# Kernel tuning notes

Hardware: AMD Instinct MI355X
Metric: run time of the kernel (lower is better)

## Reference

```python
import math
import jax, jax.numpy as jnp
import numpy as np

B, N, DQ, DK, DV, H = 8, 1024, 256, 256, 256, 8
EPS_SM = 1e-15
EPS_LN = 1e-5


def _layer_norm(x, g, b):
    mu = jnp.mean(x, axis=-1, keepdims=True)
    var = jnp.mean((x - mu) ** 2, axis=-1, keepdims=True)
    return (x - mu) * jax.lax.rsqrt(var + EPS_LN) * g + b


def setup_inputs() -> dict:
    key = jax.random.key(0)
    ks = jax.random.split(key, 16)
    s = 0.05
    inp = {
        "Q": jax.random.normal(ks[0], (B, N, DQ), jnp.float32),
        "K": jax.random.normal(ks[1], (B, N, DK), jnp.float32),
        "lengths": jnp.clip(jax.random.randint(ks[2], (B,), 0, N), 1, N),
        "Wq": jax.random.normal(ks[3], (DQ, DV), jnp.float32) * s,
        "bq": jnp.zeros((DV,), jnp.float32),
        "Wk": jax.random.normal(ks[4], (DK, DV), jnp.float32) * s,
        "bk": jnp.zeros((DV,), jnp.float32),
        "Wv": jax.random.normal(ks[5], (DK, DV), jnp.float32) * s,
        "bv": jnp.zeros((DV,), jnp.float32),
        "Wo": jax.random.normal(ks[6], (DV, DV), jnp.float32) * s,
        "bo": jnp.zeros((DV,), jnp.float32),
        "g0": jnp.ones((DV,), jnp.float32),
        "b0": jnp.zeros((DV,), jnp.float32),
        "g1": jnp.ones((DV,), jnp.float32),
        "b1": jnp.zeros((DV,), jnp.float32),
    }
    return inp


def reference(Q, K, lengths, Wq, bq, Wk, bk, Wv, bv, Wo, bo, g0, b0, g1, b1):
    d = DV // H  # head dim
    mask = (jnp.arange(N) < lengths[:, None]).astype(Q.dtype)  # (B, N)
    q = (Q @ Wq + bq) * mask[..., None]  # (B, N, DV)
    k = (K @ Wk + bk) * mask[..., None]
    v = (K @ Wv + bv) * mask[..., None]
    qh = q.reshape(B, N, H, d)
    kh = k.reshape(B, N, H, d)
    vh = v.reshape(B, N, H, d)
    # NB: original scales by sqrt(dim_V), not sqrt(head_dim)
    scores = jnp.einsum("bnhd,bmhd->bhnm", qh, kh) / math.sqrt(DV)
    # set_softmax: raw exp, mask rows and cols by lengths, normalize over keys
    e = jnp.exp(scores) * mask[:, None, :, None] * mask[:, None, None, :]
    A = e / (jnp.sum(e, axis=-1, keepdims=True) + EPS_SM)  # (B, H, N, N)
    O = qh + jnp.einsum("bhnm,bmhd->bnhd", A, vh)  # residual per head
    O = O.reshape(B, N, DV)
    O = _layer_norm(O, g0, b0)
    O = O + jax.nn.relu(O @ Wo + bo)
    O = _layer_norm(O, g1, b1)
    return O
```

## Files before the change

kernel.cpp:

```cpp
#include <hip/hip_runtime.h>
#include <hip/hip_bf16.h>


typedef __attribute__((ext_vector_type(8))) short short8;
typedef __attribute__((ext_vector_type(4))) short short4v;
typedef __attribute__((ext_vector_type(4))) float f32x4;

__device__ __forceinline__ short f2bf(float f) {
    union { float f; unsigned u; } x; x.f = f;
    unsigned r = x.u + 0x7fffu + ((x.u >> 16) & 1u);
    return (short)(r >> 16);
}
__device__ __forceinline__ float bf2f(short s) {
    union { unsigned u; float f; } x; x.u = ((unsigned)(unsigned short)s) << 16;
    return x.f;
}

__global__ __launch_bounds__(256) void wtrans_kernel(
    const float* __restrict__ Wq, const float* __restrict__ Wk,
    const float* __restrict__ Wv, const float* __restrict__ Wo,
    short* __restrict__ WqT, short* __restrict__ WkT,
    short* __restrict__ WvT, short* __restrict__ WoT)
{
    const float* W; short* T;
    switch (blockIdx.y) {
        case 0:  W = Wq; T = WqT; break;
        case 1:  W = Wk; T = WkT; break;
        case 2:  W = Wv; T = WvT; break;
        default: W = Wo; T = WoT; break;
    }
    int base = blockIdx.x * 4096 + threadIdx.x;
    #pragma unroll
    for (int i = 0; i < 16; i++) {
        int e = base + i * 256;
        int n = e >> 8, k = e & 255;
        T[e] = f2bf(W[k * 256 + n]);
    }
}

__global__ __launch_bounds__(256) void proj_kernel(
    const float* __restrict__ Q, const float* __restrict__ Kin,
    const short* __restrict__ WqT, const short* __restrict__ WkT, const short* __restrict__ WvT,
    const float* __restrict__ bq, const float* __restrict__ bk, const float* __restrict__ bv,
    const int* __restrict__ lengths,
    short* __restrict__ qb, short* __restrict__ kb, short* __restrict__ vT)
{
    const int which = blockIdx.y;
    const float* A    = (which == 0) ? Q   : Kin;
    const short* WT   = (which == 0) ? WqT : (which == 1) ? WkT : WvT;
    const float* bias = (which == 0) ? bq  : (which == 1) ? bk  : bv;

    const int tid = threadIdx.x;
    const int lane = tid & 63, wid = tid >> 6;
    const int m = lane & 15, quad = lane >> 4;
    const int rh = wid >> 1, ch = wid & 1;
    const int r0 = blockIdx.x * 32 + rh * 16;
    const int c0 = ch * 128;
    const int b = blockIdx.x >> 5;
    const int len = lengths[b];
    const int ntok0 = r0 & 1023;

    f32x4 acc[8];
    #pragma unroll
    for (int t = 0; t < 8; t++) acc[t] = (f32x4){0.f, 0.f, 0.f, 0.f};

    if (ntok0 < len) {
        const float* arow = A + (size_t)(r0 + m) * 256;
        for (int kk = 0; kk < 256; kk += 32) {
            const float* ap = arow + kk + quad * 8;
            float4 f0 = *(const float4*)(ap);
            float4 f1 = *(const float4*)(ap + 4);
            short8 af;
            af[0] = f2bf(f0.x); af[1] = f2bf(f0.y); af[2] = f2bf(f0.z); af[3] = f2bf(f0.w);
            af[4] = f2bf(f1.x); af[5] = f2bf(f1.y); af[6] = f2bf(f1.z); af[7] = f2bf(f1.w);
            #pragma unroll
            for (int t = 0; t < 8; t++) {
                short8 bf = *(const short8*)(WT + (c0 + t * 16 + m) * 256 + kk + quad * 8);
                acc[t] = __builtin_amdgcn_mfma_f32_16x16x32_bf16(af, bf, acc[t], 0, 0, 0);
            }
        }
    }

    #pragma unroll
    for (int t = 0; t < 8; t++) {
        int n = c0 + t * 16 + m;
        float bv_ = bias[n];
        int h = n >> 5, i = n & 31;
        int bh = b * 8 + h;
        #pragma unroll
        for (int reg = 0; reg < 4; reg++) {
            int ntok = ntok0 + quad * 4 + reg;
            float val = (ntok < len) ? (acc[t][reg] + bv_) : 0.f;
            short s = f2bf(val);
            if (which == 2) {
                vT[(size_t)(bh * 32 + i) * 1024 + ntok] = s;
            } else {
                short* dst = (which == 0) ? qb : kb;
                dst[((size_t)bh * 1024 + ntok) * 32 + i] = s;
            }
        }
    }
}

__global__ __launch_bounds__(256) void attn_kernel(
    const short* __restrict__ qb, const short* __restrict__ kb, const short* __restrict__ vT,
    const int* __restrict__ lengths, float* __restrict__ O1)
{
    __shared__ short P[4][16][72];
    __shared__ float cbO[2][16][33];
    __shared__ float cbL[2][16];
    const int tid = threadIdx.x;
    const int lane = tid & 63, wid = tid >> 6;
    const int m = lane & 15, quad = lane >> 4;
    const int ks = wid & 1, qh = wid >> 1;
    const int bh = blockIdx.y;
    const int b = bh >> 3, h = bh & 7;
    const int len = lengths[b];
    const int qr0 = blockIdx.x * 32 + qh * 16;

    const short* qbase = qb + (size_t)bh * 1024 * 32;
    const short* kbase = kb + (size_t)bh * 1024 * 32;
    const short* vbase = vT + (size_t)bh * 32 * 1024;

    const short8 qf = *(const short8*)(qbase + (qr0 + m) * 32 + quad * 8);

    f32x4 o0 = (f32x4){0.f, 0.f, 0.f, 0.f};
    f32x4 o1 = (f32x4){0.f, 0.f, 0.f, 0.f};
    float l[4] = {0.f, 0.f, 0.f, 0.f};

    const int kbeg = ks * 512;
    int kchunks = 0;
    if (qr0 < len && len > kbeg) {
        int rem = len - kbeg;
        kchunks = rem >= 512 ? 8 : ((rem + 63) >> 6);
    }

    for (int ci = 0; ci < kchunks; ci++) {
        int key0 = kbeg + ci * 64;
        #pragma unroll
        for (int t = 0; t < 4; t++) {
            short8 kf = *(const short8*)(kbase + (key0 + t * 16 + m) * 32 + quad * 8);
            f32x4 s = __builtin_amdgcn_mfma_f32_16x16x32_bf16(qf, kf,
                        (f32x4){0.f, 0.f, 0.f, 0.f}, 0, 0, 0);
            int col = key0 + t * 16 + m;
            bool cm = col < len;
            #pragma unroll
            for (int reg = 0; reg < 4; reg++) {
                float e = cm ? __expf(s[reg] * 0.0625f) : 0.f;
                l[reg] += e;
                P[wid][quad * 4 + reg][t * 16 + m] = f2bf(e);
            }
        }
        asm volatile("s_waitcnt lgkmcnt(0)" ::: "memory");
        #pragma unroll
        for (int c = 0; c < 2; c++) {
            short8 pf  = *(const short8*)(&P[wid][m][c * 32 + quad * 8]);
            short8 vf0 = *(const short8*)(vbase + (size_t)(m) * 1024      + key0 + c * 32 + quad * 8);
            short8 vf1 = *(const short8*)(vbase + (size_t)(16 + m) * 1024 + key0 + c * 32 + quad * 8);
            o0 = __builtin_amdgcn_mfma_f32_16x16x32_bf16(pf, vf0, o0, 0, 0, 0);
            o1 = __builtin_amdgcn_mfma_f32_16x16x32_bf16(pf, vf1, o1, 0, 0, 0);
        }
    }

    #pragma unroll
    for (int reg = 0; reg < 4; reg++) {
        float s = l[reg];
        s += __shfl_xor(s, 1); s += __shfl_xor(s, 2);
        s += __shfl_xor(s, 4); s += __shfl_xor(s, 8);
        l[reg] = s;
    }

    if (ks == 1) {
        #pragma unroll
        for (int reg = 0; reg < 4; reg++) {
            cbO[qh][quad * 4 + reg][m]      = o0[reg];
            cbO[qh][quad * 4 + reg][16 + m] = o1[reg];
        }
        if (m == 0) {
            #pragma unroll
            for (int reg = 0; reg < 4; reg++) cbL[qh][quad * 4 + reg] = l[reg];
        }
    }
    __syncthreads();
    if (ks == 0) {
        const int hbase = h * 32;
        #pragma unroll
        for (int reg = 0; reg < 4; reg++) {
            int r = quad * 4 + reg;
            o0[reg] += cbO[qh][r][m];
            o1[reg] += cbO[qh][r][16 + m];
            float lt = l[reg] + cbL[qh][r];
            int qrow = qr0 + r;
            float f = (qrow < len) ? 1.f / (lt + 1e-15f) : 0.f;
            size_t obase = ((size_t)(b * 1024 + qrow)) * 256 + hbase;
            float q0 = bf2f(qbase[qrow * 32 + m]);
            float q1 = bf2f(qbase[qrow * 32 + 16 + m]);
            O1[obase + m]      = q0 + o0[reg] * f;
            O1[obase + 16 + m] = q1 + o1[reg] * f;
        }
    }
}

__global__ __launch_bounds__(256) void ln0_kernel(
    const float* __restrict__ O1, const float* __restrict__ g0, const float* __restrict__ b0,
    short* __restrict__ Xb)
{
    const int tid = threadIdx.x;
    const int lane = tid & 63, wid = tid >> 6;
    const int token = blockIdx.x * 4 + wid;
    const float* row = O1 + (size_t)token * 256;
    float4 x = *(const float4*)(row + lane * 4);
    float s  = x.x + x.y + x.z + x.w;
    float s2 = x.x * x.x + x.y * x.y + x.z * x.z + x.w * x.w;
    #pragma unroll
    for (int msk = 1; msk < 64; msk <<= 1) {
        s  += __shfl_xor(s, msk);
        s2 += __shfl_xor(s2, msk);
    }
    float mean = s * (1.f / 256.f);
    float var  = s2 * (1.f / 256.f) - mean * mean;
    float rs = rsqrtf(var + 1e-5f);
    float4 g = *(const float4*)(g0 + lane * 4);
    float4 bb = *(const float4*)(b0 + lane * 4);
    short4v y;
    y[0] = f2bf((x.x - mean) * rs * g.x + bb.x);
    y[1] = f2bf((x.y - mean) * rs * g.y + bb.y);
    y[2] = f2bf((x.z - mean) * rs * g.z + bb.z);
    y[3] = f2bf((x.w - mean) * rs * g.w + bb.w);
    *(short4v*)(Xb + (size_t)token * 256 + lane * 4) = y;
}

__global__ __launch_bounds__(256) void out_kernel(
    const short* __restrict__ Xb, const short* __restrict__ WoT,
    const float* __restrict__ bo, const float* __restrict__ g1, const float* __restrict__ b1,
    float* __restrict__ out)
{
    __shared__ float st[2][2][2][16];
    const int tid = threadIdx.x;
    const int lane = tid & 63, wid = tid >> 6;
    const int m = lane & 15, quad = lane >> 4;
    const int rh = wid >> 1, ch = wid & 1;
    const int r0 = blockIdx.x * 32 + rh * 16;
    const int c0 = ch * 128;

    f32x4 acc[8];
    #pragma unroll
    for (int t = 0; t < 8; t++) acc[t] = (f32x4){0.f, 0.f, 0.f, 0.f};

    const short* arow = Xb + (size_t)(r0 + m) * 256;
    for (int kk = 0; kk < 256; kk += 32) {
        short8 af = *(const short8*)(arow + kk + quad * 8);
        #pragma unroll
        for (int t = 0; t < 8; t++) {
            short8 bf = *(const short8*)(WoT + (c0 + t * 16 + m) * 256 + kk + quad * 8);
            acc[t] = __builtin_amdgcn_mfma_f32_16x16x32_bf16(af, bf, acc[t], 0, 0, 0);
        }
    }

    float s1[4] = {0.f, 0.f, 0.f, 0.f};
    float s2[4] = {0.f, 0.f, 0.f, 0.f};
    #pragma unroll
    for (int t = 0; t < 8; t++) {
        int n = c0 + t * 16 + m;
        float bon = bo[n];
        #pragma unroll
        for (int reg = 0; reg < 4; reg++) {
            int token = r0 + quad * 4 + reg;
            float xv = bf2f(Xb[(size_t)token * 256 + n]);
            float c = acc[t][reg] + bon;
            float yv = xv + (c > 0.f ? c : 0.f);
            acc[t][reg] = yv;
            s1[reg] += yv;
            s2[reg] += yv * yv;
        }
    }
    #pragma unroll
    for (int reg = 0; reg < 4; reg++) {
        float a = s1[reg], bsum = s2[reg];
        a += __shfl_xor(a, 1); a += __shfl_xor(a, 2); a += __shfl_xor(a, 4); a += __shfl_xor(a, 8);
        bsum += __shfl_xor(bsum, 1); bsum += __shfl_xor(bsum, 2); bsum += __shfl_xor(bsum, 4); bsum += __shfl_xor(bsum, 8);
        s1[reg] = a; s2[reg] = bsum;
    }
    if (m == 0) {
        #pragma unroll
        for (int reg = 0; reg < 4; reg++) {
            st[rh][ch][0][quad * 4 + reg] = s1[reg];
            st[rh][ch][1][quad * 4 + reg] = s2[reg];
        }
    }
    __syncthreads();
    #pragma unroll
    for (int reg = 0; reg < 4; reg++) {
        int r = quad * 4 + reg;
        float t1 = s1[reg] + st[rh][ch ^ 1][0][r];
        float t2 = s2[reg] + st[rh][ch ^ 1][1][r];
        float mean = t1 * (1.f / 256.f);
        float var  = t2 * (1.f / 256.f) - mean * mean;
        float rs = rsqrtf(var + 1e-5f);
        int token = r0 + r;
        #pragma unroll
        for (int t = 0; t < 8; t++) {
            int n = c0 + t * 16 + m;
            out[(size_t)token * 256 + n] = (acc[t][reg] - mean) * rs * g1[n] + b1[n];
        }
    }
}

extern "C" void kernel_launch(void* const* d_in, const int* in_sizes, int n_in,
                              void* d_out, int out_size, void* d_ws, size_t ws_size,
                              hipStream_t stream) {
    const float* Q   = (const float*)d_in[0];
    const float* K   = (const float*)d_in[1];
    const int* lengths = (const int*)d_in[2];
    const float* Wq  = (const float*)d_in[3];
    const float* bq  = (const float*)d_in[4];
    const float* Wk  = (const float*)d_in[5];
    const float* bk  = (const float*)d_in[6];
    const float* Wv  = (const float*)d_in[7];
    const float* bv  = (const float*)d_in[8];
    const float* Wo  = (const float*)d_in[9];
    const float* bo  = (const float*)d_in[10];
    const float* g0  = (const float*)d_in[11];
    const float* b0  = (const float*)d_in[12];
    const float* g1  = (const float*)d_in[13];
    const float* b1  = (const float*)d_in[14];
    float* out = (float*)d_out;

    char* ws = (char*)d_ws;
    short* qb  = (short*)(ws);
    short* kb  = (short*)(ws + (4u << 20));
    short* vT  = (short*)(ws + (8u << 20));
    float* O1  = (float*)(ws + (12u << 20));
    short* Xb  = (short*)(ws + (20u << 20));
    short* WqT = (short*)(ws + (24u << 20));
    short* WkT = (short*)(ws + (24u << 20) + (128u << 10));
    short* WvT = (short*)(ws + (24u << 20) + (256u << 10));
    short* WoT = (short*)(ws + (24u << 20) + (384u << 10));

    wtrans_kernel<<<dim3(16, 4), 256, 0, stream>>>(Wq, Wk, Wv, Wo, WqT, WkT, WvT, WoT);
    proj_kernel<<<dim3(256, 3), 256, 0, stream>>>(Q, K, WqT, WkT, WvT, bq, bk, bv,
                                                  lengths, qb, kb, vT);
    attn_kernel<<<dim3(32, 64), 256, 0, stream>>>(qb, kb, vT, lengths, O1);
    ln0_kernel<<<dim3(2048), 256, 0, stream>>>(O1, g0, b0, Xb);
    out_kernel<<<dim3(256), 256, 0, stream>>>(Xb, WoT, bo, g1, b1, out);
}
```

Baseline: 167.2 us.

## Fuse LayerNorm0 into output GEMM, tile weight transpose, prefetch V in attention

Removes the separate ln0 kernel by normalizing O1 rows inside out_kernel into an LDS bf16 tile, which saves one launch and the Xb round-trip through global memory. out_kernel now handles 16 rows per block across 512 blocks, with 4 waves each covering 64 columns and the row statistics combined through shared memory. The weight-transpose kernel moves to an LDS-tiled version so both reads and writes are coalesced. In attention, V fragments are loaded at the top of each key chunk so their latency overlaps the QK and exp work, at the cost of extra registers.

```diff
diff --git a/kernel.cpp b/kernel.cpp
--- a/kernel.cpp
+++ b/kernel.cpp
@@ -22,6 +22,7 @@
     short* __restrict__ WqT, short* __restrict__ WkT,
     short* __restrict__ WvT, short* __restrict__ WoT)
 {
+    __shared__ short tile[64][72];
     const float* W; short* T;
     switch (blockIdx.y) {
         case 0:  W = Wq; T = WqT; break;
@@ -29,12 +30,20 @@
         case 2:  W = Wv; T = WvT; break;
         default: W = Wo; T = WoT; break;
     }
-    int base = blockIdx.x * 4096 + threadIdx.x;
+    const int k0 = (blockIdx.x >> 2) * 64;
+    const int n0 = (blockIdx.x & 3) * 64;
+    const int c  = threadIdx.x & 63;
+    const int r4 = threadIdx.x >> 6;
     #pragma unroll
     for (int i = 0; i < 16; i++) {
-        int e = base + i * 256;
-        int n = e >> 8, k = e & 255;
-        T[e] = f2bf(W[k * 256 + n]);
+        int k = r4 + i * 4;
+        tile[k][c] = f2bf(W[(size_t)(k0 + k) * 256 + n0 + c]);
+    }
+    __syncthreads();
+    #pragma unroll
+    for (int i = 0; i < 16; i++) {
+        int n = r4 + i * 4;
+        T[(size_t)(n0 + n) * 256 + k0 + c] = tile[c][n];
     }
 }
 
@@ -137,6 +146,10 @@
 
     for (int ci = 0; ci < kchunks; ci++) {
         int key0 = kbeg + ci * 64;
+        short8 vf0a = *(const short8*)(vbase + (size_t)(m) * 1024      + key0 + quad * 8);
+        short8 vf1a = *(const short8*)(vbase + (size_t)(16 + m) * 1024 + key0 + quad * 8);
+        short8 vf0b = *(const short8*)(vbase + (size_t)(m) * 1024      + key0 + 32 + quad * 8);
+        short8 vf1b = *(const short8*)(vbase + (size_t)(16 + m) * 1024 + key0 + 32 + quad * 8);
         #pragma unroll
         for (int t = 0; t < 4; t++) {
             short8 kf = *(const short8*)(kbase + (key0 + t * 16 + m) * 32 + quad * 8);
@@ -152,14 +165,12 @@
             }
         }
         asm volatile("s_waitcnt lgkmcnt(0)" ::: "memory");
-        #pragma unroll
-        for (int c = 0; c < 2; c++) {
-            short8 pf  = *(const short8*)(&P[wid][m][c * 32 + quad * 8]);
-            short8 vf0 = *(const short8*)(vbase + (size_t)(m) * 1024      + key0 + c * 32 + quad * 8);
-            short8 vf1 = *(const short8*)(vbase + (size_t)(16 + m) * 1024 + key0 + c * 32 + quad * 8);
-            o0 = __builtin_amdgcn_mfma_f32_16x16x32_bf16(pf, vf0, o0, 0, 0, 0);
-            o1 = __builtin_amdgcn_mfma_f32_16x16x32_bf16(pf, vf1, o1, 0, 0, 0);
-        }
+        short8 pf0 = *(const short8*)(&P[wid][m][quad * 8]);
+        short8 pf1 = *(const short8*)(&P[wid][m][32 + quad * 8]);
+        o0 = __builtin_amdgcn_mfma_f32_16x16x32_bf16(pf0, vf0a, o0, 0, 0, 0);
+        o1 = __builtin_amdgcn_mfma_f32_16x16x32_bf16(pf0, vf1a, o1, 0, 0, 0);
+        o0 = __builtin_amdgcn_mfma_f32_16x16x32_bf16(pf1, vf0b, o0, 0, 0, 0);
+        o1 = __builtin_amdgcn_mfma_f32_16x16x32_bf16(pf1, vf1b, o1, 0, 0, 0);
     }
 
     #pragma unroll
@@ -201,105 +212,128 @@
     }
 }
 
-__global__ __launch_bounds__(256) void ln0_kernel(
-    const float* __restrict__ O1, const float* __restrict__ g0, const float* __restrict__ b0,
-    short* __restrict__ Xb)
-{
-    const int tid = threadIdx.x;
-    const int lane = tid & 63, wid = tid >> 6;
-    const int token = blockIdx.x * 4 + wid;
-    const float* row = O1 + (size_t)token * 256;
-    float4 x = *(const float4*)(row + lane * 4);
-    float s  = x.x + x.y + x.z + x.w;
-    float s2 = x.x * x.x + x.y * x.y + x.z * x.z + x.w * x.w;
-    #pragma unroll
-    for (int msk = 1; msk < 64; msk <<= 1) {
-        s  += __shfl_xor(s, msk);
-        s2 += __shfl_xor(s2, msk);
-    }
-    float mean = s * (1.f / 256.f);
-    float var  = s2 * (1.f / 256.f) - mean * mean;
-    float rs = rsqrtf(var + 1e-5f);
-    float4 g = *(const float4*)(g0 + lane * 4);
-    float4 bb = *(const float4*)(b0 + lane * 4);
-    short4v y;
-    y[0] = f2bf((x.x - mean) * rs * g.x + bb.x);
-    y[1] = f2bf((x.y - mean) * rs * g.y + bb.y);
-    y[2] = f2bf((x.z - mean) * rs * g.z + bb.z);
-    y[3] = f2bf((x.w - mean) * rs * g.w + bb.w);
-    *(short4v*)(Xb + (size_t)token * 256 + lane * 4) = y;
-}
-
 __global__ __launch_bounds__(256) void out_kernel(
-    const short* __restrict__ Xb, const short* __restrict__ WoT,
+    const float* __restrict__ O1, const short* __restrict__ WoT,
+    const float* __restrict__ g0, const float* __restrict__ b0,
     const float* __restrict__ bo, const float* __restrict__ g1, const float* __restrict__ b1,
     float* __restrict__ out)
 {
-    __shared__ float st[2][2][2][16];
+    __shared__ short Xs[16][264];
+    __shared__ float st[4][2][16];
     const int tid = threadIdx.x;
+    const int r0 = blockIdx.x * 16;
+
+    {
+        const int lrow  = tid >> 4;
+        const int cbase = (tid & 15) * 16;
+        const float* rowp = O1 + (size_t)(r0 + lrow) * 256 + cbase;
+        float4 a0 = ((const float4*)rowp)[0];
+        float4 a1 = ((const float4*)rowp)[1];
+        float4 a2 = ((const float4*)rowp)[2];
+        float4 a3 = ((const float4*)rowp)[3];
+        float s  = a0.x + a0.y + a0.z + a0.w + a1.x + a1.y + a1.z + a1.w
+                 + a2.x + a2.y + a2.z + a2.w + a3.x + a3.y + a3.z + a3.w;
+        float s2 = a0.x*a0.x + a0.y*a0.y + a0.z*a0.z + a0.w*a0.w
+                 + a1.x*a1.x + a1.y*a1.y + a1.z*a1.z + a1.w*a1.w
+                 + a2.x*a2.x + a2.y*a2.y + a2.z*a2.z + a2.w*a2.w
+                 + a3.x*a3.x + a3.y*a3.y + a3.z*a3.z + a3.w*a3.w;
+        s  += __shfl_xor(s, 1);  s  += __shfl_xor(s, 2);
+        s  += __shfl_xor(s, 4);  s  += __shfl_xor(s, 8);
+        s2 += __shfl_xor(s2, 1); s2 += __shfl_xor(s2, 2);
+        s2 += __shfl_xor(s2, 4); s2 += __shfl_xor(s2, 8);
+        float mean = s * (1.f / 256.f);
+        float var  = s2 * (1.f / 256.f) - mean * mean;
+        float rs = rsqrtf(var + 1e-5f);
+        float4 g0a = ((const float4*)(g0 + cbase))[0];
+        float4 g0b = ((const float4*)(g0 + cbase))[1];
+        float4 g0c = ((const float4*)(g0 + cbase))[2];
+        float4 g0d = ((const float4*)(g0 + cbase))[3];
+        float4 b0a = ((const float4*)(b0 + cbase))[0];
+        float4 b0b = ((const float4*)(b0 + cbase))[1];
+        float4 b0c = ((const float4*)(b0 + cbase))[2];
+        float4 b0d = ((const float4*)(b0 + cbase))[3];
+        short8 y0, y1;
+        y0[0] = f2bf((a0.x - mean) * rs * g0a.x + b0a.x);
+        y0[1] = f2bf((a0.y - mean) * rs * g0a.y + b0a.y);
+        y0[2] = f2bf((a0.z - mean) * rs * g0a.z + b0a.z);
+        y0[3] = f2bf((a0.w - mean) * rs * g0a.w + b0a.w);
+        y0[4] = f2bf((a1.x - mean) * rs * g0b.x + b0b.x);
+        y0[5] = f2bf((a1.y - mean) * rs * g0b.y + b0b.y);
+        y0[6] = f2bf((a1.z - mean) * rs * g0b.z + b0b.z);
+        y0[7] = f2bf((a1.w - mean) * rs * g0b.w + b0b.w);
+        y1[0] = f2bf((a2.x - mean) * rs * g0c.x + b0c.x);
+        y1[1] = f2bf((a2.y - mean) * rs * g0c.y + b0c.y);
+        y1[2] = f2bf((a2.z - mean) * rs * g0c.z + b0c.z);
+        y1[3] = f2bf((a2.w - mean) * rs * g0c.w + b0c.w);
+        y1[4] = f2bf((a3.x - mean) * rs * g0d.x + b0d.x);
+        y1[5] = f2bf((a3.y - mean) * rs * g0d.y + b0d.y);
+        y1[6] = f2bf((a3.z - mean) * rs * g0d.z + b0d.z);
+        y1[7] = f2bf((a3.w - mean) * rs * g0d.w + b0d.w);
+        *(short8*)(&Xs[lrow][cbase])     = y0;
+        *(short8*)(&Xs[lrow][cbase + 8]) = y1;
+    }
+    __syncthreads();
+
     const int lane = tid & 63, wid = tid >> 6;
     const int m = lane & 15, quad = lane >> 4;
-    const int rh = wid >> 1, ch = wid & 1;
-    const int r0 = blockIdx.x * 32 + rh * 16;
-    const int c0 = ch * 128;
-
-    f32x4 acc[8];
-    #pragma unroll
-    for (int t = 0; t < 8; t++) acc[t] = (f32x4){0.f, 0.f, 0.f, 0.f};
-
-    const short* arow = Xb + (size_t)(r0 + m) * 256;
+    const int c0 = wid * 64;
+
+    f32x4 acc[4];
+    #pragma unroll
+    for (int t = 0; t < 4; t++) acc[t] = (f32x4){0.f, 0.f, 0.f, 0.f};
+
     for (int kk = 0; kk < 256; kk += 32) {
-        short8 af = *(const short8*)(arow + kk + quad * 8);
-        #pragma unroll
-        for (int t = 0; t < 8; t++) {
+        short8 af = *(const short8*)(&Xs[m][kk + quad * 8]);
+        #pragma unroll
+        for (int t = 0; t < 4; t++) {
             short8 bf = *(const short8*)(WoT + (c0 + t * 16 + m) * 256 + kk + quad * 8);
             acc[t] = __builtin_amdgcn_mfma_f32_16x16x32_bf16(af, bf, acc[t], 0, 0, 0);
         }
     }
 
     float s1[4] = {0.f, 0.f, 0.f, 0.f};
-    float s2[4] = {0.f, 0.f, 0.f, 0.f};
-    #pragma unroll
-    for (int t = 0; t < 8; t++) {
+    float s2v[4] = {0.f, 0.f, 0.f, 0.f};
+    #pragma unroll
+    for (int t = 0; t < 4; t++) {
         int n = c0 + t * 16 + m;
         float bon = bo[n];
         #pragma unroll
         for (int reg = 0; reg < 4; reg++) {
-            int token = r0 + quad * 4 + reg;
-            float xv = bf2f(Xb[(size_t)token * 256 + n]);
+            int r = quad * 4 + reg;
+            float xv = bf2f(Xs[r][n]);
             float c = acc[t][reg] + bon;
             float yv = xv + (c > 0.f ? c : 0.f);
             acc[t][reg] = yv;
             s1[reg] += yv;
-            s2[reg] += yv * yv;
+            s2v[reg] += yv * yv;
         }
     }
     #pragma unroll
     for (int reg = 0; reg < 4; reg++) {
-        float a = s1[reg], bsum = s2[reg];
+        float a = s1[reg], bsum = s2v[reg];
         a += __shfl_xor(a, 1); a += __shfl_xor(a, 2); a += __shfl_xor(a, 4); a += __shfl_xor(a, 8);
         bsum += __shfl_xor(bsum, 1); bsum += __shfl_xor(bsum, 2); bsum += __shfl_xor(bsum, 4); bsum += __shfl_xor(bsum, 8);
-        s1[reg] = a; s2[reg] = bsum;
+        s1[reg] = a; s2v[reg] = bsum;
     }
     if (m == 0) {
         #pragma unroll
         for (int reg = 0; reg < 4; reg++) {
-            st[rh][ch][0][quad * 4 + reg] = s1[reg];
-            st[rh][ch][1][quad * 4 + reg] = s2[reg];
+            st[wid][0][quad * 4 + reg] = s1[reg];
+            st[wid][1][quad * 4 + reg] = s2v[reg];
         }
     }
     __syncthreads();
     #pragma unroll
     for (int reg = 0; reg < 4; reg++) {
         int r = quad * 4 + reg;
-        float t1 = s1[reg] + st[rh][ch ^ 1][0][r];
-        float t2 = s2[reg] + st[rh][ch ^ 1][1][r];
+        float t1 = st[0][0][r] + st[1][0][r] + st[2][0][r] + st[3][0][r];
+        float t2 = st[0][1][r] + st[1][1][r] + st[2][1][r] + st[3][1][r];
         float mean = t1 * (1.f / 256.f);
         float var  = t2 * (1.f / 256.f) - mean * mean;
         float rs = rsqrtf(var + 1e-5f);
         int token = r0 + r;
         #pragma unroll
-        for (int t = 0; t < 8; t++) {
+        for (int t = 0; t < 4; t++) {
             int n = c0 + t * 16 + m;
             out[(size_t)token * 256 + n] = (acc[t][reg] - mean) * rs * g1[n] + b1[n];
         }
@@ -331,16 +365,14 @@
     short* kb  = (short*)(ws + (4u << 20));
     short* vT  = (short*)(ws + (8u << 20));
     float* O1  = (float*)(ws + (12u << 20));
-    short* Xb  = (short*)(ws + (20u << 20));
-    short* WqT = (short*)(ws + (24u << 20));
-    short* WkT = (short*)(ws + (24u << 20) + (128u << 10));
-    short* WvT = (short*)(ws + (24u << 20) + (256u << 10));
-    short* WoT = (short*)(ws + (24u << 20) + (384u << 10));
+    short* WqT = (short*)(ws + (20u << 20));
+    short* WkT = (short*)(ws + (20u << 20) + (128u << 10));
+    short* WvT = (short*)(ws + (20u << 20) + (256u << 10));
+    short* WoT = (short*)(ws + (20u << 20) + (384u << 10));
 
     wtrans_kernel<<<dim3(16, 4), 256, 0, stream>>>(Wq, Wk, Wv, Wo, WqT, WkT, WvT, WoT);
     proj_kernel<<<dim3(256, 3), 256, 0, stream>>>(Q, K, WqT, WkT, WvT, bq, bk, bv,
                                                   lengths, qb, kb, vT);
     attn_kernel<<<dim3(32, 64), 256, 0, stream>>>(qb, kb, vT, lengths, O1);
-    ln0_kernel<<<dim3(2048), 256, 0, stream>>>(O1, g0, b0, Xb);
-    out_kernel<<<dim3(256), 256, 0, stream>>>(Xb, WoT, bo, g1, b1, out);
-}
+    out_kernel<<<dim3(512), 256, 0, stream>>>(O1, WoT, g0, b0, bo, g1, b1, out);
+}
```

Result: no change. 164.0 us (-1.9%).
